# Optimization experiments

Hardware: AMD Instinct MI355X
Metric: run time of the kernel (lower is better)

The kernel has to match this reference:

```python
import math
import jax, jax.numpy as jnp
import numpy as np

B, S, D, H = 4, 1024, 768, 12  # batch, seq, hidden, heads (ViT-Base)
HD = D // H                     # head size = 64
EPS = 1e-12                     # F.normalize eps


def setup_inputs() -> dict:
    key = jax.random.key(0)
    ks = jax.random.split(key, 7)
    s = 0.02
    return {
        "hidden_states": jax.random.normal(ks[0], (B, S, D), dtype=jnp.float32),
        "Wq": jax.random.normal(ks[1], (D, D), dtype=jnp.float32) * s,
        "bq": jax.random.normal(ks[2], (D,), dtype=jnp.float32) * s,
        "Wv": jax.random.normal(ks[3], (D, D), dtype=jnp.float32) * s,
        "bv": jax.random.normal(ks[4], (D,), dtype=jnp.float32) * s,
        "Wo": jax.random.normal(ks[5], (D, D), dtype=jnp.float32) * s,
        "bo": jax.random.normal(ks[6], (D,), dtype=jnp.float32) * s,
    }


def _split_heads(x):
    # [B,S,D] -> [B,H,S,hd]
    b, s, _ = x.shape
    return x.reshape(b, s, H, HD).transpose(0, 2, 1, 3)


def reference(hidden_states, Wq, bq, Wv, bv, Wo, bo):
    b, s, d_model = hidden_states.shape
    # Linear layers (torch Linear: x @ W^T + b; here W stored already transposed)
    mixed_q = hidden_states @ Wq + bq          # key == query in this module
    mixed_v = hidden_states @ Wv + bv
    q = _split_heads(mixed_q)                  # [B,H,S,hd]
    v = _split_heads(mixed_v)                  # [B,H,S,hd]

    # symmetric self-attention (Q @ Q^T)
    scores = jnp.einsum("bhsd,bhtd->bhst", q, q) / math.sqrt(HD)
    probs1 = jax.nn.softmax(scores, axis=-1)                 # [B,H,S,S]
    probs = 0.5 * (probs1 + probs1.transpose(0, 1, 3, 2))    # symmetrize

    # F.normalize(value_layer, dim=2): L2-normalize along the SEQUENCE axis
    vnorm = jnp.maximum(jnp.sqrt(jnp.sum(v * v, axis=2, keepdims=True)), EPS)
    V = v / vnorm                                            # [B,H,S,hd]

    # random-walk Laplacian: D^{-1}(D - P) = I - P / rowsum  (diag structure exploited,
    # same math as diag_embed + matmul in the original)
    dvec = probs.sum(axis=3)                                 # [B,H,S]
    Pn = probs / dvec[..., :, None]                          # D^{-1} P
    LrwV = V - jnp.einsum("bhst,bhtd->bhsd", Pn, V)          # L_rw @ V

    # trace( sum_{b,h} V^T L_rw V ) = sum over all (b,h,s,d) of V * (L_rw V)
    denom = jnp.float32(HD * H * b)
    tr = jnp.abs(jnp.sum(V * LrwV)) / denom

    # orthogonality regularizer: sum (V^T V - I)^2
    VtV = jnp.einsum("bhsd,bhse->bhde", V, V)                # [B,H,hd,hd]
    regular_term = jnp.sum((VtV - jnp.eye(HD, dtype=V.dtype)) ** 2) / denom

    # context = P @ V  (is_last=False)
    ctx = jnp.einsum("bhst,bhtd->bhsd", probs, v)
    ctx = ctx.transpose(0, 2, 1, 3).reshape(b, s, d_model)
    attention_output = ctx @ Wo + bo                         # dropout = identity (p=0)
    return (attention_output, tr, regular_term, mixed_q, mixed_q)
```

## Files before the change

### kernel.cpp

```cpp
#include <hip/hip_runtime.h>
#include <math.h>

constexpr float SCALE = 0.125f;

typedef __attribute__((ext_vector_type(8))) short bf8;
typedef __attribute__((ext_vector_type(8))) unsigned short u16x8;
typedef __attribute__((ext_vector_type(4))) float f32x4;

static __device__ __forceinline__ unsigned short f2bf(float f) {
    unsigned int u = __float_as_uint(f);
    u += 0x7fffu + ((u >> 16) & 1u);
    return (unsigned short)(u >> 16);
}
static __device__ __forceinline__ float bf2f(unsigned short h) {
    return __uint_as_float(((unsigned int)h) << 16);
}
static __device__ __forceinline__ bf8 ld8(const unsigned short* p) {
    return *reinterpret_cast<const bf8*>(p);
}
static __device__ __forceinline__ unsigned int cvtpk(float lo, float hi) {
    unsigned int r;
    asm("v_cvt_pk_bf16_f32 %0, %1, %2" : "=v"(r) : "v"(lo), "v"(hi));
    return r;
}

__global__ __launch_bounds__(256)
void k_prep(const float* __restrict__ Wq, const float* __restrict__ Wv,
            unsigned short* __restrict__ WTq, unsigned short* __restrict__ WTv)
{
    __shared__ unsigned short T[64 * 72];
    const int bid = blockIdx.x;
    const bool isQ = (bid < 144);
    const int lb = isQ ? bid : bid - 144;
    const float* __restrict__ W = isQ ? Wq : Wv;
    unsigned short* __restrict__ WT = isQ ? WTq : WTv;
    const int n0 = (lb % 12) * 64;
    const int k0 = (lb / 12) * 64;
    const int tid = threadIdx.x;
    const int r  = tid >> 2;
    const int c0 = (tid & 3) * 16;
    const float* src = &W[(size_t)(k0 + r) * 768 + n0 + c0];
    #pragma unroll
    for (int q = 0; q < 4; ++q) {
        const float4 v = *reinterpret_cast<const float4*>(src + q * 4);
        uint2 pk;
        pk.x = cvtpk(v.x, v.y);
        pk.y = cvtpk(v.z, v.w);
        *reinterpret_cast<uint2*>(&T[r * 72 + c0 + q * 4]) = pk;
    }
    __syncthreads();
    const int n  = tid >> 2;
    const int kc = (tid & 3) * 16;
    u16x8 o0, o1;
    #pragma unroll
    for (int i = 0; i < 8; ++i) o0[i] = T[(kc + i) * 72 + n];
    #pragma unroll
    for (int i = 0; i < 8; ++i) o1[i] = T[(kc + 8 + i) * 72 + n];
    unsigned short* dst = WT + (size_t)(n0 + n) * 768 + k0 + kc;
    *reinterpret_cast<u16x8*>(dst)     = o0;
    *reinterpret_cast<u16x8*>(dst + 8) = o1;
}

__global__ __launch_bounds__(256)
void k_wt(const float* __restrict__ W, unsigned short* __restrict__ WT)
{
    __shared__ unsigned short T[64 * 72];
    const int n0 = blockIdx.x * 64;
    const int k0 = blockIdx.y * 64;
    const int tid = threadIdx.x;
    const int r  = tid >> 2;
    const int c0 = (tid & 3) * 16;
    const float* src = &W[(size_t)(k0 + r) * 768 + n0 + c0];
    #pragma unroll
    for (int q = 0; q < 4; ++q) {
        const float4 v = *reinterpret_cast<const float4*>(src + q * 4);
        uint2 pk;
        pk.x = cvtpk(v.x, v.y);
        pk.y = cvtpk(v.z, v.w);
        *reinterpret_cast<uint2*>(&T[r * 72 + c0 + q * 4]) = pk;
    }
    __syncthreads();
    const int n  = tid >> 2;
    const int kc = (tid & 3) * 16;
    u16x8 o0, o1;
    #pragma unroll
    for (int i = 0; i < 8; ++i) o0[i] = T[(kc + i) * 72 + n];
    #pragma unroll
    for (int i = 0; i < 8; ++i) o1[i] = T[(kc + 8 + i) * 72 + n];
    unsigned short* dst = WT + (size_t)(n0 + n) * 768 + k0 + kc;
    *reinterpret_cast<u16x8*>(dst)     = o0;
    *reinterpret_cast<u16x8*>(dst + 8) = o1;
}

__global__ __launch_bounds__(256)
void k_gemm_qv(const float* __restrict__ X,
               const unsigned short* __restrict__ WTq,
               const unsigned short* __restrict__ WTv,
               const float* __restrict__ bq, const float* __restrict__ bv,
               float* __restrict__ mq1, float* __restrict__ mq2,
               unsigned short* __restrict__ qb, unsigned short* __restrict__ mvb)
{
    __shared__ unsigned short As[64 * 72];
    __shared__ unsigned short Bs[128 * 72];
    const int m0 = blockIdx.x * 64;
    const bool isQ = (blockIdx.y < 6);
    const int n0 = (isQ ? blockIdx.y : blockIdx.y - 6) * 128;
    const unsigned short* __restrict__ WT = isQ ? WTq : WTv;
    const float* __restrict__ bias = isQ ? bq : bv;
    const int tid = threadIdx.x;
    const int wave = tid >> 6, lane = tid & 63, lm = lane & 15, lg = lane >> 4;
    const int wn = wave;

    f32x4 acc[4][2];
    #pragma unroll
    for (int mi = 0; mi < 4; ++mi)
        #pragma unroll
        for (int ni = 0; ni < 2; ++ni) acc[mi][ni] = (f32x4){0.f, 0.f, 0.f, 0.f};

    for (int k0 = 0; k0 < 768; k0 += 64) {
        #pragma unroll
        for (int it = 0; it < 4; ++it) {
            const int idx = tid + it * 256;
            const int arow = idx >> 4;
            const int ac4  = (idx & 15) * 4;
            const float4 v = *reinterpret_cast<const float4*>(
                &X[(size_t)(m0 + arow) * 768 + k0 + ac4]);
            uint2 pk;
            pk.x = cvtpk(v.x, v.y);
            pk.y = cvtpk(v.z, v.w);
            *reinterpret_cast<uint2*>(&As[arow * 72 + ac4]) = pk;
            const int brow = idx >> 3;
            const int bc8  = (idx & 7) * 8;
            *reinterpret_cast<u16x8*>(&Bs[brow * 72 + bc8]) =
                *reinterpret_cast<const u16x8*>(&WT[(size_t)(n0 + brow) * 768 + k0 + bc8]);
        }
        __syncthreads();
        #pragma unroll
        for (int ks = 0; ks < 2; ++ks) {
            bf8 af[4], bfr[2];
            #pragma unroll
            for (int mi = 0; mi < 4; ++mi)
                af[mi] = *reinterpret_cast<const bf8*>(
                    &As[(mi * 16 + lm) * 72 + ks * 32 + lg * 8]);
            #pragma unroll
            for (int ni = 0; ni < 2; ++ni)
                bfr[ni] = *reinterpret_cast<const bf8*>(
                    &Bs[(wn * 32 + ni * 16 + lm) * 72 + ks * 32 + lg * 8]);
            #pragma unroll
            for (int mi = 0; mi < 4; ++mi)
                #pragma unroll
                for (int ni = 0; ni < 2; ++ni)
                    acc[mi][ni] = __builtin_amdgcn_mfma_f32_16x16x32_bf16(
                        af[mi], bfr[ni], acc[mi][ni], 0, 0, 0);
        }
        __syncthreads();
    }
    #pragma unroll
    for (int ni = 0; ni < 2; ++ni) {
        const int c = n0 + wn * 32 + ni * 16 + lm;
        const float bcol = bias[c];
        #pragma unroll
        for (int mi = 0; mi < 4; ++mi)
            #pragma unroll
            for (int j = 0; j < 4; ++j) {
                const int r = m0 + mi * 16 + lg * 4 + j;
                const float v = acc[mi][ni][j] + bcol;
                const size_t off = (size_t)r * 768 + c;
                if (isQ) {
                    mq1[off] = v;
                    mq2[off] = v;
                    qb[off]  = f2bf(v);
                } else {
                    mvb[off] = f2bf(v);
                }
            }
    }
}

__global__ __launch_bounds__(256)
void k_gemm_one(const unsigned short* __restrict__ Xb,
                const unsigned short* __restrict__ WT,
                const float* __restrict__ bias, float* __restrict__ out)
{
    __shared__ unsigned short As[64 * 72];
    __shared__ unsigned short Bs[64 * 72];
    const int m0 = blockIdx.x * 64;
    const int n0 = blockIdx.y * 64;
    const int tid = threadIdx.x;
    const int w = tid >> 6, lane = tid & 63, lm = lane & 15, lg = lane >> 4;

    f32x4 acc[4];
    #pragma unroll
    for (int ni = 0; ni < 4; ++ni) acc[ni] = (f32x4){0.f, 0.f, 0.f, 0.f};

    for (int k0 = 0; k0 < 768; k0 += 64) {
        #pragma unroll
        for (int it = 0; it < 2; ++it) {
            const int idx = tid + it * 256;
            const int row = idx >> 3;
            const int c8  = (idx & 7) * 8;
            *reinterpret_cast<u16x8*>(&As[row * 72 + c8]) =
                *reinterpret_cast<const u16x8*>(&Xb[(size_t)(m0 + row) * 768 + k0 + c8]);
            *reinterpret_cast<u16x8*>(&Bs[row * 72 + c8]) =
                *reinterpret_cast<const u16x8*>(&WT[(size_t)(n0 + row) * 768 + k0 + c8]);
        }
        __syncthreads();
        #pragma unroll
        for (int ks = 0; ks < 2; ++ks) {
            const bf8 af = *reinterpret_cast<const bf8*>(
                &As[(w * 16 + lm) * 72 + ks * 32 + lg * 8]);
            #pragma unroll
            for (int ni = 0; ni < 4; ++ni) {
                const bf8 bfr = *reinterpret_cast<const bf8*>(
                    &Bs[(ni * 16 + lm) * 72 + ks * 32 + lg * 8]);
                acc[ni] = __builtin_amdgcn_mfma_f32_16x16x32_bf16(af, bfr, acc[ni], 0, 0, 0);
            }
        }
        __syncthreads();
    }
    #pragma unroll
    for (int ni = 0; ni < 4; ++ni) {
        const int c = n0 + ni * 16 + lm;
        const float bcol = bias[c];
        #pragma unroll
        for (int j = 0; j < 4; ++j) {
            const int r = m0 + w * 16 + lg * 4 + j;
            out[(size_t)r * 768 + c] = acc[ni][j] + bcol;
        }
    }
}

__global__ __launch_bounds__(256)
void k_pass1T(const unsigned short* __restrict__ qb,
              const unsigned short* __restrict__ mvb,
              unsigned short* __restrict__ vT,
              float* __restrict__ a, float* __restrict__ nrmp)
{
    __shared__ __align__(16) unsigned short Kb[2][64 * 72];
    const int bid = blockIdx.x;
    const int st = (bid >> 3) & 15;
    const int bh = (bid & 7) + 8 * (bid >> 7);
    const int b = bh / 12, h = bh % 12;
    const int s0 = st * 64;
    const int tid = threadIdx.x;
    const int w = tid >> 6, lane = tid & 63, lm = lane & 15, lg = lane >> 4;
    const size_t qoff = (size_t)(b * 1024) * 768 + h * 64;

    {
        const int r  = tid >> 2;
        const int c0 = (tid & 3) * 16;
        const unsigned short* src = mvb + (size_t)(b * 1024 + s0 + r) * 768 + h * 64 + c0;
        const u16x8 x0 = *reinterpret_cast<const u16x8*>(src);
        const u16x8 x1 = *reinterpret_cast<const u16x8*>(src + 8);
        *reinterpret_cast<u16x8*>(&Kb[0][r * 72 + c0])     = x0;
        *reinterpret_cast<u16x8*>(&Kb[0][r * 72 + c0 + 8]) = x1;
        __syncthreads();
        const int dd  = tid >> 2;
        const int sc0 = (tid & 3) * 16;
        u16x8 o0, o1;
        float ps = 0.f;
        #pragma unroll
        for (int k = 0; k < 8; ++k) {
            o0[k] = Kb[0][(sc0 + k) * 72 + dd];
            const float v = bf2f(o0[k]);
            ps = fmaf(v, v, ps);
        }
        #pragma unroll
        for (int k = 0; k < 8; ++k) {
            o1[k] = Kb[0][(sc0 + 8 + k) * 72 + dd];
            const float v = bf2f(o1[k]);
            ps = fmaf(v, v, ps);
        }
        ps += __shfl_xor(ps, 1);
        ps += __shfl_xor(ps, 2);
        if ((tid & 3) == 0) nrmp[(size_t)(bh * 16 + st) * 64 + dd] = ps;
        unsigned short* dst = vT + (size_t)bh * 65536 + (size_t)dd * 1024 + s0 + sc0;
        *reinterpret_cast<u16x8*>(dst)     = o0;
        *reinterpret_cast<u16x8*>(dst + 8) = o1;
        __syncthreads();
    }

    const unsigned short* srow_p = qb + qoff + (size_t)(s0 + 16 * w + lm) * 768;
    const bf8 qs0 = ld8(srow_p + 8 * lg);
    const bf8 qs1 = ld8(srow_p + 32 + 8 * lg);
    const f32x4 z = {0.f, 0.f, 0.f, 0.f};
    float r = 0.f;
    const int sr = tid >> 2;
    const int sc = (tid & 3) << 4;

    u16x8 kr0 = *reinterpret_cast<const u16x8*>(qb + qoff + (size_t)sr * 768 + sc);
    u16x8 kr1 = *reinterpret_cast<const u16x8*>(qb + qoff + (size_t)sr * 768 + sc + 8);
    *reinterpret_cast<u16x8*>(&Kb[0][sr * 72 + sc])     = kr0;
    *reinterpret_cast<u16x8*>(&Kb[0][sr * 72 + sc + 8]) = kr1;
    __syncthreads();
    int cur = 0;

    for (int tt = 0; tt < 16; ++tt) {
        if (tt < 15) {
            const size_t rg = qoff + (size_t)((tt + 1) * 64 + sr) * 768 + sc;
            kr0 = *reinterpret_cast<const u16x8*>(qb + rg);
            kr1 = *reinterpret_cast<const u16x8*>(qb + rg + 8);
        }
        #pragma unroll
        for (int nf = 0; nf < 4; ++nf) {
            const bf8 ka0 = *reinterpret_cast<const bf8*>(
                &Kb[cur][(16 * nf + lm) * 72 + 8 * lg]);
            const bf8 ka1 = *reinterpret_cast<const bf8*>(
                &Kb[cur][(16 * nf + lm) * 72 + 32 + 8 * lg]);
            f32x4 ef = __builtin_amdgcn_mfma_f32_16x16x32_bf16(ka0, qs0, z, 0, 0, 0);
            ef = __builtin_amdgcn_mfma_f32_16x16x32_bf16(ka1, qs1, ef, 0, 0, 0);
            r += __expf(ef[0] * SCALE) + __expf(ef[1] * SCALE)
               + __expf(ef[2] * SCALE) + __expf(ef[3] * SCALE);
        }
        if (tt < 15) {
            *reinterpret_cast<u16x8*>(&Kb[cur ^ 1][sr * 72 + sc])     = kr0;
            *reinterpret_cast<u16x8*>(&Kb[cur ^ 1][sr * 72 + sc + 8]) = kr1;
        }
        __syncthreads();
        cur ^= 1;
    }
    r += __shfl_xor(r, 16);
    r += __shfl_xor(r, 32);
    if (lg == 0) a[(size_t)bh * 1024 + s0 + 16 * w + lm] = 1.f / r;
}

__global__ __launch_bounds__(256)
void k_normfin(const float* __restrict__ nrmp, float* __restrict__ inv_n,
               float* __restrict__ t1p)
{
    const int bh = blockIdx.x;
    const int tid = threadIdx.x;
    __shared__ float t1s[64];
    if (tid < 64) {
        float s = 0.f;
        for (int st = 0; st < 16; ++st)
            s += nrmp[(size_t)(bh * 16 + st) * 64 + tid];
        const float n = fmaxf(sqrtf(s), 1e-12f);
        const float iv = 1.f / n;
        inv_n[bh * 64 + tid] = iv;
        t1s[tid] = s * iv * iv;
    }
    __syncthreads();
    if (tid == 0) {
        float t = 0.f;
        for (int k = 0; k < 64; ++k) t += t1s[k];
        t1p[bh] = t;
    }
}

__global__ __launch_bounds__(256)
void k_pass2(const unsigned short* __restrict__ qb,
             const unsigned short* __restrict__ vT,
             const unsigned short* __restrict__ mvb,
             const float* __restrict__ a,
             const float* __restrict__ invn,
             unsigned short* __restrict__ ctxb,
             float* __restrict__ t2p)
{
    __shared__ __align__(16) unsigned short Kb[2][64 * 72];
    __shared__ __align__(16) unsigned short Vb[2][64 * 72];
    __shared__ __align__(16) unsigned short F_lds[4 * 16 * 72];
    __shared__ float red[256];
    const int bid = blockIdx.x;
    const int st = (bid >> 3) & 15;
    const int bh = (bid & 7) + 8 * (bid >> 7);
    const int b = bh / 12, h = bh % 12;
    const int s0 = st * 64;
    const int tid = threadIdx.x;
    const int w = tid >> 6, lane = tid & 63, lm = lane & 15, lg = lane >> 4;
    const size_t qoff = (size_t)(b * 1024) * 768 + h * 64;
    const unsigned short* srow_p = qb + qoff + (size_t)(s0 + 16 * w + lm) * 768;
    const bf8 qs0 = ld8(srow_p + 8 * lg);
    const bf8 qs1 = ld8(srow_p + 32 + 8 * lg);
    const unsigned short* vbase = vT + (size_t)bh * 65536;
    const float* abase = a + (size_t)bh * 1024;
    const float a_s = abase[s0 + 16 * w + lm];
    unsigned short* Frow = &F_lds[w * 1152 + lm * 72];
    float inv2[4];
    #pragma unroll
    for (int nf = 0; nf < 4; ++nf) {
        const float iv = invn[bh * 64 + lm + 16 * nf];
        inv2[nf] = iv * iv;
    }
    const f32x4 z = {0.f, 0.f, 0.f, 0.f};
    f32x4 acc[4];
    #pragma unroll
    for (int nf = 0; nf < 4; ++nf) acc[nf] = z;
    float sF = 0.f;
    const int sr = tid >> 2;
    const int sc = (tid & 3) << 4;

    u16x8 kr0 = *reinterpret_cast<const u16x8*>(qb + qoff + (size_t)sr * 768 + sc);
    u16x8 kr1 = *reinterpret_cast<const u16x8*>(qb + qoff + (size_t)sr * 768 + sc + 8);
    u16x8 vr0 = *reinterpret_cast<const u16x8*>(vbase + (size_t)sr * 1024 + sc);
    u16x8 vr1 = *reinterpret_cast<const u16x8*>(vbase + (size_t)sr * 1024 + sc + 8);
    *reinterpret_cast<u16x8*>(&Kb[0][sr * 72 + sc])     = kr0;
    *reinterpret_cast<u16x8*>(&Kb[0][sr * 72 + sc + 8]) = kr1;
    *reinterpret_cast<u16x8*>(&Vb[0][sr * 72 + sc])     = vr0;
    *reinterpret_cast<u16x8*>(&Vb[0][sr * 72 + sc + 8]) = vr1;
    __syncthreads();
    int cur = 0;

    for (int tt = 0; tt < 16; ++tt) {
        const int t0 = tt * 64;
        if (tt < 15) {
            const size_t kg = qoff + (size_t)(t0 + 64 + sr) * 768 + sc;
            kr0 = *reinterpret_cast<const u16x8*>(qb + kg);
            kr1 = *reinterpret_cast<const u16x8*>(qb + kg + 8);
            const size_t vg = (size_t)sr * 1024 + t0 + 64 + sc;
            vr0 = *reinterpret_cast<const u16x8*>(vbase + vg);
            vr1 = *reinterpret_cast<const u16x8*>(vbase + vg + 8);
        }
        f32x4 ef[4];
        #pragma unroll
        for (int nf = 0; nf < 4; ++nf) {
            const bf8 ka0 = *reinterpret_cast<const bf8*>(
                &Kb[cur][(16 * nf + lm) * 72 + 8 * lg]);
            const bf8 ka1 = *reinterpret_cast<const bf8*>(
                &Kb[cur][(16 * nf + lm) * 72 + 32 + 8 * lg]);
            ef[nf] = __builtin_amdgcn_mfma_f32_16x16x32_bf16(ka0, qs0, z, 0, 0, 0);
            ef[nf] = __builtin_amdgcn_mfma_f32_16x16x32_bf16(ka1, qs1, ef[nf], 0, 0, 0);
        }
        #pragma unroll
        for (int nf = 0; nf < 4; ++nf) {
            const float4 af = *reinterpret_cast<const float4*>(
                abase + t0 + 16 * nf + 4 * lg);
            const float f0 = __expf(ef[nf][0] * SCALE) * (a_s + af.x);
            const float f1 = __expf(ef[nf][1] * SCALE) * (a_s + af.y);
            const float f2 = __expf(ef[nf][2] * SCALE) * (a_s + af.z);
            const float f3 = __expf(ef[nf][3] * SCALE) * (a_s + af.w);
            sF += (f0 + f1) + (f2 + f3);
            uint2 pk;
            pk.x = cvtpk(f0, f1);
            pk.y = cvtpk(f2, f3);
            *reinterpret_cast<uint2*>(&Frow[16 * nf + 4 * lg]) = pk;
        }
        #pragma unroll
        for (int ks = 0; ks < 2; ++ks) {
            const bf8 fa = *reinterpret_cast<const bf8*>(&Frow[32 * ks + 8 * lg]);
            #pragma unroll
            for (int nf = 0; nf < 4; ++nf) {
                const bf8 vfr = *reinterpret_cast<const bf8*>(
                    &Vb[cur][(16 * nf + lm) * 72 + 32 * ks + 8 * lg]);
                acc[nf] = __builtin_amdgcn_mfma_f32_16x16x32_bf16(fa, vfr, acc[nf], 0, 0, 0);
            }
        }
        if (tt < 15) {
            *reinterpret_cast<u16x8*>(&Kb[cur ^ 1][sr * 72 + sc])     = kr0;
            *reinterpret_cast<u16x8*>(&Kb[cur ^ 1][sr * 72 + sc + 8]) = kr1;
            *reinterpret_cast<u16x8*>(&Vb[cur ^ 1][sr * 72 + sc])     = vr0;
            *reinterpret_cast<u16x8*>(&Vb[cur ^ 1][sr * 72 + sc + 8]) = vr1;
        }
        __syncthreads();
        cur ^= 1;
    }
    sF += __shfl_xor(sF, 16);
    sF += __shfl_xor(sF, 32);

    float t2 = 0.f;
    #pragma unroll
    for (int j = 0; j < 4; ++j) {
        const int srow = s0 + 16 * w + 4 * lg + j;
        const float sFj = __shfl(sF, 4 * lg + j);
        const float rdv = 2.f / sFj;
        const size_t rowoff = (size_t)(b * 1024 + srow) * 768 + h * 64;
        #pragma unroll
        for (int nf = 0; nf < 4; ++nf) {
            const int d = lm + 16 * nf;
            const float cf = 0.5f * acc[nf][j];
            ctxb[rowoff + d] = f2bf(cf);
            const float vv = bf2f(mvb[rowoff + d]);
            t2 = fmaf(vv * cf, inv2[nf] * rdv, t2);
        }
    }
    red[tid] = t2;
    __syncthreads();
    for (int k = 128; k >= 1; k >>= 1) {
        if (tid < k) red[tid] += red[tid + k];
        __syncthreads();
    }
    if (tid == 0) t2p[bh * 16 + st] = red[0];
}

__global__ __launch_bounds__(256)
void k_reg(const unsigned short* __restrict__ vT, float* __restrict__ Gpart)
{
    const int bh = blockIdx.x;
    const int q  = blockIdx.y;
    const int tid = threadIdx.x;
    const int w = tid >> 6, lane = tid & 63, lm = lane & 15, lg = lane >> 4;
    const unsigned short* base = vT + (size_t)bh * 65536;
    const unsigned short* arowp = base + (size_t)(16 * w + lm) * 1024;
    const f32x4 z = {0.f, 0.f, 0.f, 0.f};
    f32x4 acc[4];
    #pragma unroll
    for (int nf = 0; nf < 4; ++nf) acc[nf] = z;
    #pragma unroll
    for (int kk = 0; kk < 4; ++kk) {
        const int t0 = (q * 4 + kk) * 32 + 8 * lg;
        const bf8 av = ld8(arowp + t0);
        #pragma unroll
        for (int nf = 0; nf < 4; ++nf) {
            const bf8 bv = ld8(base + (size_t)(lm + 16 * nf) * 1024 + t0);
            acc[nf] = __builtin_amdgcn_mfma_f32_16x16x32_bf16(av, bv, acc[nf], 0, 0, 0);
        }
    }
    float* gdst = Gpart + (size_t)(bh * 8 + q) * 4096;
    #pragma unroll
    for (int nf = 0; nf < 4; ++nf) {
        const int d2 = lm + 16 * nf;
        #pragma unroll
        for (int j = 0; j < 4; ++j) {
            const int d1 = 16 * w + 4 * lg + j;
            gdst[d1 * 64 + d2] = acc[nf][j];
        }
    }
}

__global__ __launch_bounds__(256)
void k_regfin(const float* __restrict__ Gpart, const float* __restrict__ invn,
              float* __restrict__ regp)
{
    const int bh = blockIdx.x;
    const int tid = threadIdx.x;
    float part = 0.f;
    for (int c = tid; c < 4096; c += 256) {
        const int d1 = c >> 6, d2 = c & 63;
        float g = 0.f;
        #pragma unroll
        for (int q = 0; q < 8; ++q)
            g += Gpart[(size_t)(bh * 8 + q) * 4096 + c];
        g *= invn[bh * 64 + d1] * invn[bh * 64 + d2];
        const float diff = g - ((d1 == d2) ? 1.f : 0.f);
        part = fmaf(diff, diff, part);
    }
    __shared__ float red[256];
    red[tid] = part;
    __syncthreads();
    for (int k = 128; k >= 1; k >>= 1) {
        if (tid < k) red[tid] += red[tid + k];
        __syncthreads();
    }
    if (tid == 0) regp[bh] = red[0];
}

__global__ __launch_bounds__(256)
void k_final(const float* __restrict__ t1p, const float* __restrict__ t2p,
             const float* __restrict__ regp, float* __restrict__ out_tr,
             float* __restrict__ out_reg)
{
    const int tid = threadIdx.x;
    float s1 = 0.f, s2 = 0.f, s3 = 0.f;
    for (int i = tid; i < 768; i += 256) s2 += t2p[i];
    if (tid < 48) { s1 = t1p[tid]; s3 = regp[tid]; }
    __shared__ float R1[256];
    __shared__ float R2[256];
    __shared__ float R3[256];
    R1[tid] = s1; R2[tid] = s2; R3[tid] = s3;
    __syncthreads();
    for (int w = 128; w >= 1; w >>= 1) {
        if (tid < w) { R1[tid] += R1[tid + w]; R2[tid] += R2[tid + w]; R3[tid] += R3[tid + w]; }
        __syncthreads();
    }
    if (tid == 0) {
        *out_tr  = fabsf(R1[0] - R2[0]) / 3072.f;
        *out_reg = R3[0] / 3072.f;
    }
}

extern "C" void kernel_launch(void* const* d_in, const int* in_sizes, int n_in,
                              void* d_out, int out_size, void* d_ws, size_t ws_size,
                              hipStream_t stream)
{
    const float* X  = (const float*)d_in[0];
    const float* Wq = (const float*)d_in[1];
    const float* bq = (const float*)d_in[2];
    const float* Wv = (const float*)d_in[3];
    const float* bv = (const float*)d_in[4];
    const float* Wo = (const float*)d_in[5];
    const float* bo = (const float*)d_in[6];

    float* out = (float*)d_out;
    float* att = out;
    float* tr  = out + 3145728;
    float* rg  = out + 3145729;
    float* mq1 = out + 3145730;
    float* mq2 = out + 6291458;

    float* ws = (float*)d_ws;
    unsigned short* mvb  = (unsigned short*)(ws);
    unsigned short* qb   = (unsigned short*)(ws + 1572864);
    float*          Gpart = ws + 1572864;
    unsigned short* vTslot = (unsigned short*)(ws + 3145728);
    unsigned short* WTq  = vTslot;
    unsigned short* WTv  = vTslot + 589824;
    unsigned short* vT   = vTslot;
    unsigned short* WTo  = vTslot;
    unsigned short* ctxb = (unsigned short*)(ws + 4718592);
    float* nrmp = ws + 6291456;
    float* aarr = ws + 6389760;
    float* invn = ws + 6438960;
    float* t1p  = ws + 6442032;
    float* t2p  = ws + 6442080;
    float* regp = ws + 6442848;

    if (ws_size < (size_t)6442896 * sizeof(float)) return;

    k_prep     <<<288,          256, 0, stream>>>(Wq, Wv, WTq, WTv);
    k_gemm_qv  <<<dim3(64, 12), 256, 0, stream>>>(X, WTq, WTv, bq, bv, mq1, mq2, qb, mvb);
    k_pass1T   <<<768,          256, 0, stream>>>(qb, mvb, vT, aarr, nrmp);
    k_normfin  <<<48,           256, 0, stream>>>(nrmp, invn, t1p);
    k_pass2    <<<768,          256, 0, stream>>>(qb, vT, mvb, aarr, invn, ctxb, t2p);
    k_reg      <<<dim3(48, 8),  256, 0, stream>>>(vT, Gpart);
    k_wt       <<<dim3(12, 12), 256, 0, stream>>>(Wo, WTo);
    k_regfin   <<<48,           256, 0, stream>>>(Gpart, invn, regp);
    k_gemm_one <<<dim3(64, 12), 256, 0, stream>>>(ctxb, WTo, bo, att);
    k_final    <<<1,            256, 0, stream>>>(t1p, t2p, regp, tr, rg);
}
```

Before: 124.1 us.

## Split key tiles across waves and keep probability fragments in registers

In pass1 and pass2, each wave now handles a 16-key slice of every key tile for all 64 query rows, instead of owning 16 query rows and walking all keys. This lets each wave load its K fragment once and reuse it across four query subtiles. In pass2 the bf16 probability fragments are assembled directly in registers from two consecutive key tiles, which removes the F_lds round trip. V uses a triple-buffered LDS ring, and the partial context results from the four waves are reduced through LDS before vectorized ctx stores. The costs are 64 accumulator registers per thread, an extra cross-wave reduction and more barriers, with launch bounds set to 3 blocks per CU.

```diff
diff --git a/kernel.cpp b/kernel.cpp
--- a/kernel.cpp
+++ b/kernel.cpp
@@ -6,6 +6,7 @@
 typedef __attribute__((ext_vector_type(8))) short bf8;
 typedef __attribute__((ext_vector_type(8))) unsigned short u16x8;
 typedef __attribute__((ext_vector_type(4))) float f32x4;
+typedef __attribute__((ext_vector_type(4))) unsigned int u32x4;
 
 static __device__ __forceinline__ unsigned short f2bf(float f) {
     unsigned int u = __float_as_uint(f);
@@ -22,6 +23,11 @@
     unsigned int r;
     asm("v_cvt_pk_bf16_f32 %0, %1, %2" : "=v"(r) : "v"(lo), "v"(hi));
     return r;
+}
+static __device__ __forceinline__ bf8 frag_from(unsigned int d0, unsigned int d1,
+                                                unsigned int d2, unsigned int d3) {
+    u32x4 t; t[0] = d0; t[1] = d1; t[2] = d2; t[3] = d3;
+    return __builtin_bit_cast(bf8, t);
 }
 
 __global__ __launch_bounds__(256)
@@ -237,6 +243,7 @@
               float* __restrict__ a, float* __restrict__ nrmp)
 {
     __shared__ __align__(16) unsigned short Kb[2][64 * 72];
+    __shared__ float rred[4][4][16];
     const int bid = blockIdx.x;
     const int st = (bid >> 3) & 15;
     const int bh = (bid & 7) + 8 * (bid >> 7);
@@ -280,48 +287,65 @@
         __syncthreads();
     }
 
-    const unsigned short* srow_p = qb + qoff + (size_t)(s0 + 16 * w + lm) * 768;
-    const bf8 qs0 = ld8(srow_p + 8 * lg);
-    const bf8 qs1 = ld8(srow_p + 32 + 8 * lg);
+    bf8 qs0[4], qs1[4];
+    #pragma unroll
+    for (int si = 0; si < 4; ++si) {
+        const unsigned short* sp = qb + qoff + (size_t)(s0 + 16 * si + lm) * 768;
+        qs0[si] = ld8(sp + 8 * lg);
+        qs1[si] = ld8(sp + 32 + 8 * lg);
+    }
     const f32x4 z = {0.f, 0.f, 0.f, 0.f};
-    float r = 0.f;
+    float rs[4] = {0.f, 0.f, 0.f, 0.f};
     const int sr = tid >> 2;
-    const int sc = (tid & 3) << 4;
-
-    u16x8 kr0 = *reinterpret_cast<const u16x8*>(qb + qoff + (size_t)sr * 768 + sc);
-    u16x8 kr1 = *reinterpret_cast<const u16x8*>(qb + qoff + (size_t)sr * 768 + sc + 8);
-    *reinterpret_cast<u16x8*>(&Kb[0][sr * 72 + sc])     = kr0;
-    *reinterpret_cast<u16x8*>(&Kb[0][sr * 72 + sc + 8]) = kr1;
-    __syncthreads();
-    int cur = 0;
-
-    for (int tt = 0; tt < 16; ++tt) {
-        if (tt < 15) {
-            const size_t rg = qoff + (size_t)((tt + 1) * 64 + sr) * 768 + sc;
-            kr0 = *reinterpret_cast<const u16x8*>(qb + rg);
-            kr1 = *reinterpret_cast<const u16x8*>(qb + rg + 8);
-        }
-        #pragma unroll
-        for (int nf = 0; nf < 4; ++nf) {
-            const bf8 ka0 = *reinterpret_cast<const bf8*>(
-                &Kb[cur][(16 * nf + lm) * 72 + 8 * lg]);
-            const bf8 ka1 = *reinterpret_cast<const bf8*>(
-                &Kb[cur][(16 * nf + lm) * 72 + 32 + 8 * lg]);
-            f32x4 ef = __builtin_amdgcn_mfma_f32_16x16x32_bf16(ka0, qs0, z, 0, 0, 0);
-            ef = __builtin_amdgcn_mfma_f32_16x16x32_bf16(ka1, qs1, ef, 0, 0, 0);
-            r += __expf(ef[0] * SCALE) + __expf(ef[1] * SCALE)
-               + __expf(ef[2] * SCALE) + __expf(ef[3] * SCALE);
-        }
-        if (tt < 15) {
-            *reinterpret_cast<u16x8*>(&Kb[cur ^ 1][sr * 72 + sc])     = kr0;
-            *reinterpret_cast<u16x8*>(&Kb[cur ^ 1][sr * 72 + sc + 8]) = kr1;
-        }
-        __syncthreads();
-        cur ^= 1;
-    }
-    r += __shfl_xor(r, 16);
-    r += __shfl_xor(r, 32);
-    if (lg == 0) a[(size_t)bh * 1024 + s0 + 16 * w + lm] = 1.f / r;
+    const int sc_ = (tid & 3) << 4;
+    const int krow = (16 * w + lm) * 72;
+
+    {
+        const u16x8 k0 = *reinterpret_cast<const u16x8*>(qb + qoff + (size_t)sr * 768 + sc_);
+        const u16x8 k1 = *reinterpret_cast<const u16x8*>(qb + qoff + (size_t)sr * 768 + sc_ + 8);
+        *reinterpret_cast<u16x8*>(&Kb[0][sr * 72 + sc_])     = k0;
+        *reinterpret_cast<u16x8*>(&Kb[0][sr * 72 + sc_ + 8]) = k1;
+    }
+    __syncthreads();
+
+    for (int c = 0; c < 16; ++c) {
+        u16x8 k0, k1;
+        const bool pf = (c < 15);
+        if (pf) {
+            const size_t rg = qoff + (size_t)((c + 1) * 64 + sr) * 768 + sc_;
+            k0 = *reinterpret_cast<const u16x8*>(qb + rg);
+            k1 = *reinterpret_cast<const u16x8*>(qb + rg + 8);
+        }
+        const bf8 ka0 = *reinterpret_cast<const bf8*>(&Kb[c & 1][krow + 8 * lg]);
+        const bf8 ka1 = *reinterpret_cast<const bf8*>(&Kb[c & 1][krow + 32 + 8 * lg]);
+        #pragma unroll
+        for (int si = 0; si < 4; ++si) {
+            f32x4 ef = __builtin_amdgcn_mfma_f32_16x16x32_bf16(ka0, qs0[si], z, 0, 0, 0);
+            ef = __builtin_amdgcn_mfma_f32_16x16x32_bf16(ka1, qs1[si], ef, 0, 0, 0);
+            rs[si] += __expf(ef[0] * SCALE) + __expf(ef[1] * SCALE)
+                    + __expf(ef[2] * SCALE) + __expf(ef[3] * SCALE);
+        }
+        if (pf) {
+            *reinterpret_cast<u16x8*>(&Kb[(c + 1) & 1][sr * 72 + sc_])     = k0;
+            *reinterpret_cast<u16x8*>(&Kb[(c + 1) & 1][sr * 72 + sc_ + 8]) = k1;
+        }
+        __syncthreads();
+    }
+    #pragma unroll
+    for (int si = 0; si < 4; ++si) {
+        rs[si] += __shfl_xor(rs[si], 16);
+        rs[si] += __shfl_xor(rs[si], 32);
+    }
+    if (lane < 16) {
+        #pragma unroll
+        for (int si = 0; si < 4; ++si) rred[w][si][lm] = rs[si];
+    }
+    __syncthreads();
+    if (tid < 64) {
+        const int si = tid >> 4, l = tid & 15;
+        const float r = rred[0][si][l] + rred[1][si][l] + rred[2][si][l] + rred[3][si][l];
+        a[(size_t)bh * 1024 + s0 + tid] = 1.f / r;
+    }
 }
 
 __global__ __launch_bounds__(256)
@@ -348,7 +372,7 @@
     }
 }
 
-__global__ __launch_bounds__(256)
+__global__ __launch_bounds__(256, 3)
 void k_pass2(const unsigned short* __restrict__ qb,
              const unsigned short* __restrict__ vT,
              const unsigned short* __restrict__ mvb,
@@ -358,8 +382,8 @@
              float* __restrict__ t2p)
 {
     __shared__ __align__(16) unsigned short Kb[2][64 * 72];
-    __shared__ __align__(16) unsigned short Vb[2][64 * 72];
-    __shared__ __align__(16) unsigned short F_lds[4 * 16 * 72];
+    __shared__ __align__(16) unsigned short Vb[3][64 * 72];
+    __shared__ float sFred[4][4][16];
     __shared__ float red[256];
     const int bid = blockIdx.x;
     const int st = (bid >> 3) & 15;
@@ -369,110 +393,202 @@
     const int tid = threadIdx.x;
     const int w = tid >> 6, lane = tid & 63, lm = lane & 15, lg = lane >> 4;
     const size_t qoff = (size_t)(b * 1024) * 768 + h * 64;
-    const unsigned short* srow_p = qb + qoff + (size_t)(s0 + 16 * w + lm) * 768;
-    const bf8 qs0 = ld8(srow_p + 8 * lg);
-    const bf8 qs1 = ld8(srow_p + 32 + 8 * lg);
     const unsigned short* vbase = vT + (size_t)bh * 65536;
     const float* abase = a + (size_t)bh * 1024;
-    const float a_s = abase[s0 + 16 * w + lm];
-    unsigned short* Frow = &F_lds[w * 1152 + lm * 72];
-    float inv2[4];
-    #pragma unroll
-    for (int nf = 0; nf < 4; ++nf) {
-        const float iv = invn[bh * 64 + lm + 16 * nf];
-        inv2[nf] = iv * iv;
+
+    bf8 qs0[4], qs1[4];
+    float a_s[4];
+    #pragma unroll
+    for (int si = 0; si < 4; ++si) {
+        const unsigned short* sp = qb + qoff + (size_t)(s0 + 16 * si + lm) * 768;
+        qs0[si] = ld8(sp + 8 * lg);
+        qs1[si] = ld8(sp + 32 + 8 * lg);
+        a_s[si] = abase[s0 + 16 * si + lm];
     }
     const f32x4 z = {0.f, 0.f, 0.f, 0.f};
-    f32x4 acc[4];
-    #pragma unroll
-    for (int nf = 0; nf < 4; ++nf) acc[nf] = z;
-    float sF = 0.f;
+    f32x4 acc[4][4];
+    #pragma unroll
+    for (int si = 0; si < 4; ++si)
+        #pragma unroll
+        for (int dj = 0; dj < 4; ++dj) acc[si][dj] = z;
+    float sFr[4] = {0.f, 0.f, 0.f, 0.f};
+    unsigned int pa0[4], pa1[4], pa2[4], pa3[4];
+
     const int sr = tid >> 2;
-    const int sc = (tid & 3) << 4;
-
-    u16x8 kr0 = *reinterpret_cast<const u16x8*>(qb + qoff + (size_t)sr * 768 + sc);
-    u16x8 kr1 = *reinterpret_cast<const u16x8*>(qb + qoff + (size_t)sr * 768 + sc + 8);
-    u16x8 vr0 = *reinterpret_cast<const u16x8*>(vbase + (size_t)sr * 1024 + sc);
-    u16x8 vr1 = *reinterpret_cast<const u16x8*>(vbase + (size_t)sr * 1024 + sc + 8);
-    *reinterpret_cast<u16x8*>(&Kb[0][sr * 72 + sc])     = kr0;
-    *reinterpret_cast<u16x8*>(&Kb[0][sr * 72 + sc + 8]) = kr1;
-    *reinterpret_cast<u16x8*>(&Vb[0][sr * 72 + sc])     = vr0;
-    *reinterpret_cast<u16x8*>(&Vb[0][sr * 72 + sc + 8]) = vr1;
-    __syncthreads();
-    int cur = 0;
-
-    for (int tt = 0; tt < 16; ++tt) {
-        const int t0 = tt * 64;
-        if (tt < 15) {
-            const size_t kg = qoff + (size_t)(t0 + 64 + sr) * 768 + sc;
-            kr0 = *reinterpret_cast<const u16x8*>(qb + kg);
-            kr1 = *reinterpret_cast<const u16x8*>(qb + kg + 8);
-            const size_t vg = (size_t)sr * 1024 + t0 + 64 + sc;
-            vr0 = *reinterpret_cast<const u16x8*>(vbase + vg);
-            vr1 = *reinterpret_cast<const u16x8*>(vbase + vg + 8);
-        }
-        f32x4 ef[4];
-        #pragma unroll
-        for (int nf = 0; nf < 4; ++nf) {
-            const bf8 ka0 = *reinterpret_cast<const bf8*>(
-                &Kb[cur][(16 * nf + lm) * 72 + 8 * lg]);
-            const bf8 ka1 = *reinterpret_cast<const bf8*>(
-                &Kb[cur][(16 * nf + lm) * 72 + 32 + 8 * lg]);
-            ef[nf] = __builtin_amdgcn_mfma_f32_16x16x32_bf16(ka0, qs0, z, 0, 0, 0);
-            ef[nf] = __builtin_amdgcn_mfma_f32_16x16x32_bf16(ka1, qs1, ef[nf], 0, 0, 0);
-        }
-        #pragma unroll
-        for (int nf = 0; nf < 4; ++nf) {
-            const float4 af = *reinterpret_cast<const float4*>(
-                abase + t0 + 16 * nf + 4 * lg);
-            const float f0 = __expf(ef[nf][0] * SCALE) * (a_s + af.x);
-            const float f1 = __expf(ef[nf][1] * SCALE) * (a_s + af.y);
-            const float f2 = __expf(ef[nf][2] * SCALE) * (a_s + af.z);
-            const float f3 = __expf(ef[nf][3] * SCALE) * (a_s + af.w);
-            sF += (f0 + f1) + (f2 + f3);
-            uint2 pk;
-            pk.x = cvtpk(f0, f1);
-            pk.y = cvtpk(f2, f3);
-            *reinterpret_cast<uint2*>(&Frow[16 * nf + 4 * lg]) = pk;
-        }
-        #pragma unroll
-        for (int ks = 0; ks < 2; ++ks) {
-            const bf8 fa = *reinterpret_cast<const bf8*>(&Frow[32 * ks + 8 * lg]);
-            #pragma unroll
-            for (int nf = 0; nf < 4; ++nf) {
-                const bf8 vfr = *reinterpret_cast<const bf8*>(
-                    &Vb[cur][(16 * nf + lm) * 72 + 32 * ks + 8 * lg]);
-                acc[nf] = __builtin_amdgcn_mfma_f32_16x16x32_bf16(fa, vfr, acc[nf], 0, 0, 0);
+    const int sc_ = (tid & 3) << 4;
+    const int krow = (16 * w + lm) * 72;
+    const int vcol = 16 * w + 4 * lg;
+
+    {
+        const u16x8 k0 = *reinterpret_cast<const u16x8*>(qb + qoff + (size_t)sr * 768 + sc_);
+        const u16x8 k1 = *reinterpret_cast<const u16x8*>(qb + qoff + (size_t)sr * 768 + sc_ + 8);
+        const u16x8 v0 = *reinterpret_cast<const u16x8*>(vbase + (size_t)sr * 1024 + sc_);
+        const u16x8 v1 = *reinterpret_cast<const u16x8*>(vbase + (size_t)sr * 1024 + sc_ + 8);
+        *reinterpret_cast<u16x8*>(&Kb[0][sr * 72 + sc_])     = k0;
+        *reinterpret_cast<u16x8*>(&Kb[0][sr * 72 + sc_ + 8]) = k1;
+        *reinterpret_cast<u16x8*>(&Vb[0][sr * 72 + sc_])     = v0;
+        *reinterpret_cast<u16x8*>(&Vb[0][sr * 72 + sc_ + 8]) = v1;
+    }
+    __syncthreads();
+
+    for (int i = 0; i < 8; ++i) {
+        const int cA = 2 * i, cB = 2 * i + 1;
+        const int bA = cA % 3, bB = cB % 3, bN = (cB + 1) % 3;
+        {
+            const int t0 = cA * 64;
+            const size_t kg = qoff + (size_t)(t0 + 64 + sr) * 768 + sc_;
+            const u16x8 k0 = *reinterpret_cast<const u16x8*>(qb + kg);
+            const u16x8 k1 = *reinterpret_cast<const u16x8*>(qb + kg + 8);
+            const size_t vg = (size_t)sr * 1024 + t0 + 64 + sc_;
+            const u16x8 v0 = *reinterpret_cast<const u16x8*>(vbase + vg);
+            const u16x8 v1 = *reinterpret_cast<const u16x8*>(vbase + vg + 8);
+            const bf8 ka0 = *reinterpret_cast<const bf8*>(&Kb[0][krow + 8 * lg]);
+            const bf8 ka1 = *reinterpret_cast<const bf8*>(&Kb[0][krow + 32 + 8 * lg]);
+            const float4 at = *reinterpret_cast<const float4*>(abase + t0 + vcol);
+            #pragma unroll
+            for (int si = 0; si < 4; ++si) {
+                f32x4 ef = __builtin_amdgcn_mfma_f32_16x16x32_bf16(ka0, qs0[si], z, 0, 0, 0);
+                ef = __builtin_amdgcn_mfma_f32_16x16x32_bf16(ka1, qs1[si], ef, 0, 0, 0);
+                const float f0 = __expf(ef[0] * SCALE) * (a_s[si] + at.x);
+                const float f1 = __expf(ef[1] * SCALE) * (a_s[si] + at.y);
+                const float f2 = __expf(ef[2] * SCALE) * (a_s[si] + at.z);
+                const float f3 = __expf(ef[3] * SCALE) * (a_s[si] + at.w);
+                sFr[si] += (f0 + f1) + (f2 + f3);
+                pa0[si] = cvtpk(f0, f1);
+                pa1[si] = cvtpk(f2, f3);
             }
-        }
-        if (tt < 15) {
-            *reinterpret_cast<u16x8*>(&Kb[cur ^ 1][sr * 72 + sc])     = kr0;
-            *reinterpret_cast<u16x8*>(&Kb[cur ^ 1][sr * 72 + sc + 8]) = kr1;
-            *reinterpret_cast<u16x8*>(&Vb[cur ^ 1][sr * 72 + sc])     = vr0;
-            *reinterpret_cast<u16x8*>(&Vb[cur ^ 1][sr * 72 + sc + 8]) = vr1;
-        }
-        __syncthreads();
-        cur ^= 1;
-    }
-    sF += __shfl_xor(sF, 16);
-    sF += __shfl_xor(sF, 32);
-
+            *reinterpret_cast<u16x8*>(&Kb[1][sr * 72 + sc_])      = k0;
+            *reinterpret_cast<u16x8*>(&Kb[1][sr * 72 + sc_ + 8])  = k1;
+            *reinterpret_cast<u16x8*>(&Vb[bB][sr * 72 + sc_])     = v0;
+            *reinterpret_cast<u16x8*>(&Vb[bB][sr * 72 + sc_ + 8]) = v1;
+        }
+        __syncthreads();
+        {
+            const int t0 = cB * 64;
+            u16x8 k0, k1, v0, v1;
+            const bool pf = (cB < 15);
+            if (pf) {
+                const size_t kg = qoff + (size_t)(t0 + 64 + sr) * 768 + sc_;
+                k0 = *reinterpret_cast<const u16x8*>(qb + kg);
+                k1 = *reinterpret_cast<const u16x8*>(qb + kg + 8);
+                const size_t vg = (size_t)sr * 1024 + t0 + 64 + sc_;
+                v0 = *reinterpret_cast<const u16x8*>(vbase + vg);
+                v1 = *reinterpret_cast<const u16x8*>(vbase + vg + 8);
+            }
+            const bf8 ka0 = *reinterpret_cast<const bf8*>(&Kb[1][krow + 8 * lg]);
+            const bf8 ka1 = *reinterpret_cast<const bf8*>(&Kb[1][krow + 32 + 8 * lg]);
+            const float4 at = *reinterpret_cast<const float4*>(abase + t0 + vcol);
+            #pragma unroll
+            for (int si = 0; si < 4; ++si) {
+                f32x4 ef = __builtin_amdgcn_mfma_f32_16x16x32_bf16(ka0, qs0[si], z, 0, 0, 0);
+                ef = __builtin_amdgcn_mfma_f32_16x16x32_bf16(ka1, qs1[si], ef, 0, 0, 0);
+                const float f0 = __expf(ef[0] * SCALE) * (a_s[si] + at.x);
+                const float f1 = __expf(ef[1] * SCALE) * (a_s[si] + at.y);
+                const float f2 = __expf(ef[2] * SCALE) * (a_s[si] + at.z);
+                const float f3 = __expf(ef[3] * SCALE) * (a_s[si] + at.w);
+                sFr[si] += (f0 + f1) + (f2 + f3);
+                pa2[si] = cvtpk(f0, f1);
+                pa3[si] = cvtpk(f2, f3);
+            }
+            #pragma unroll
+            for (int dj = 0; dj < 4; ++dj) {
+                const uint2 vA = *reinterpret_cast<const uint2*>(
+                    &Vb[bA][(16 * dj + lm) * 72 + vcol]);
+                const uint2 vB = *reinterpret_cast<const uint2*>(
+                    &Vb[bB][(16 * dj + lm) * 72 + vcol]);
+                const bf8 bfr = frag_from(vA.x, vA.y, vB.x, vB.y);
+                #pragma unroll
+                for (int si = 0; si < 4; ++si) {
+                    const bf8 af = frag_from(pa0[si], pa1[si], pa2[si], pa3[si]);
+                    acc[si][dj] = __builtin_amdgcn_mfma_f32_16x16x32_bf16(
+                        af, bfr, acc[si][dj], 0, 0, 0);
+                }
+            }
+            if (pf) {
+                *reinterpret_cast<u16x8*>(&Kb[0][sr * 72 + sc_])      = k0;
+                *reinterpret_cast<u16x8*>(&Kb[0][sr * 72 + sc_ + 8])  = k1;
+                *reinterpret_cast<u16x8*>(&Vb[bN][sr * 72 + sc_])     = v0;
+                *reinterpret_cast<u16x8*>(&Vb[bN][sr * 72 + sc_ + 8]) = v1;
+            }
+        }
+        __syncthreads();
+    }
+
+    #pragma unroll
+    for (int si = 0; si < 4; ++si) {
+        sFr[si] += __shfl_xor(sFr[si], 16);
+        sFr[si] += __shfl_xor(sFr[si], 32);
+    }
+    if (lane < 16) {
+        #pragma unroll
+        for (int si = 0; si < 4; ++si) sFred[w][si][lm] = sFr[si];
+    }
+
+    float* ctxA = reinterpret_cast<float*>(&Kb[0][0]);
+    float* ctxB = reinterpret_cast<float*>(&Vb[0][0]);
+    if (w == 0) {
+        #pragma unroll
+        for (int si = 0; si < 4; ++si)
+            #pragma unroll
+            for (int dj = 0; dj < 4; ++dj)
+                #pragma unroll
+                for (int j = 0; j < 4; ++j)
+                    ctxA[(16 * si + 4 * lg + j) * 68 + 16 * dj + lm] = acc[si][dj][j];
+    } else if (w == 1) {
+        #pragma unroll
+        for (int si = 0; si < 4; ++si)
+            #pragma unroll
+            for (int dj = 0; dj < 4; ++dj)
+                #pragma unroll
+                for (int j = 0; j < 4; ++j)
+                    ctxB[(16 * si + 4 * lg + j) * 68 + 16 * dj + lm] = acc[si][dj][j];
+    }
+    __syncthreads();
+    if (w == 2) {
+        #pragma unroll
+        for (int si = 0; si < 4; ++si)
+            #pragma unroll
+            for (int dj = 0; dj < 4; ++dj)
+                #pragma unroll
+                for (int j = 0; j < 4; ++j)
+                    ctxA[(16 * si + 4 * lg + j) * 68 + 16 * dj + lm] += acc[si][dj][j];
+    } else if (w == 3) {
+        #pragma unroll
+        for (int si = 0; si < 4; ++si)
+            #pragma unroll
+            for (int dj = 0; dj < 4; ++dj)
+                #pragma unroll
+                for (int j = 0; j < 4; ++j)
+                    ctxB[(16 * si + 4 * lg + j) * 68 + 16 * dj + lm] += acc[si][dj][j];
+    }
+    __syncthreads();
+
+    const int es  = tid >> 2;
+    const int ed0 = (tid & 3) * 16;
+    const float sFt = sFred[0][es >> 4][es & 15] + sFred[1][es >> 4][es & 15]
+                    + sFred[2][es >> 4][es & 15] + sFred[3][es >> 4][es & 15];
+    const float rdv = 2.f / sFt;
+    const size_t rowoff = (size_t)(b * 1024 + s0 + es) * 768 + h * 64 + ed0;
+    const u16x8 mv0 = *reinterpret_cast<const u16x8*>(mvb + rowoff);
+    const u16x8 mv1 = *reinterpret_cast<const u16x8*>(mvb + rowoff + 8);
     float t2 = 0.f;
-    #pragma unroll
-    for (int j = 0; j < 4; ++j) {
-        const int srow = s0 + 16 * w + 4 * lg + j;
-        const float sFj = __shfl(sF, 4 * lg + j);
-        const float rdv = 2.f / sFj;
-        const size_t rowoff = (size_t)(b * 1024 + srow) * 768 + h * 64;
-        #pragma unroll
-        for (int nf = 0; nf < 4; ++nf) {
-            const int d = lm + 16 * nf;
-            const float cf = 0.5f * acc[nf][j];
-            ctxb[rowoff + d] = f2bf(cf);
-            const float vv = bf2f(mvb[rowoff + d]);
-            t2 = fmaf(vv * cf, inv2[nf] * rdv, t2);
-        }
-    }
+    u16x8 o0, o1;
+    #pragma unroll
+    for (int jj = 0; jj < 8; ++jj) {
+        const float cv = 0.5f * (ctxA[es * 68 + ed0 + jj] + ctxB[es * 68 + ed0 + jj]);
+        o0[jj] = f2bf(cv);
+        const float iv = invn[bh * 64 + ed0 + jj];
+        t2 = fmaf(bf2f(mv0[jj]) * cv, iv * iv * rdv, t2);
+    }
+    #pragma unroll
+    for (int jj = 0; jj < 8; ++jj) {
+        const float cv = 0.5f * (ctxA[es * 68 + ed0 + 8 + jj] + ctxB[es * 68 + ed0 + 8 + jj]);
+        o1[jj] = f2bf(cv);
+        const float iv = invn[bh * 64 + ed0 + 8 + jj];
+        t2 = fmaf(bf2f(mv1[jj]) * cv, iv * iv * rdv, t2);
+    }
+    *reinterpret_cast<u16x8*>(ctxb + rowoff)     = o0;
+    *reinterpret_cast<u16x8*>(ctxb + rowoff + 8) = o1;
     red[tid] = t2;
     __syncthreads();
     for (int k = 128; k >= 1; k >>= 1) {
```

Result: slower. 151.7 us (+22.3%).
